# Performance work log

Measured on AMD Instinct MI355X. Metric: run time of the kernel, lower is better.

## Reference

```python
import jax, jax.numpy as jnp
import numpy as np

B, T, DM = 2, 2048, 2048
HQ, HKV, D = 16, 4, 128
MULT = 0.08838834764831845  # attn_output_multiplier = 1/sqrt(key_size)
ROPE_BASE = 10000.0


def rotate_half(x):
    x1, x2 = jnp.split(x, 2, axis=-1)
    return jnp.concatenate((-x2, x1), axis=-1)


def rope_tables(seq_len, dim, dtype):
    inv_freq = 1.0 / (ROPE_BASE ** (jnp.arange(0, dim, 2, dtype=jnp.float32) / dim))
    t = jnp.arange(seq_len, dtype=jnp.float32)
    freqs = jnp.outer(t, inv_freq)              # [T, D/2]
    emb = jnp.concatenate((freqs, freqs), axis=-1)  # [T, D]
    cos = jnp.cos(emb)[None, :, None, :].astype(dtype)  # [1, T, 1, D]
    sin = jnp.sin(emb)[None, :, None, :].astype(dtype)
    return cos, sin


def setup_inputs() -> dict:
    key = jax.random.key(0)
    ks = jax.random.split(key, 5)
    s = 1.0 / np.sqrt(DM)
    x = jax.random.normal(ks[0], (B, T, DM), dtype=jnp.float32)
    Wq = jax.random.normal(ks[1], (DM, HQ * D), dtype=jnp.float32) * s
    Wk = jax.random.normal(ks[2], (DM, HKV * D), dtype=jnp.float32) * s
    Wv = jax.random.normal(ks[3], (DM, HKV * D), dtype=jnp.float32) * s
    Wo = jax.random.normal(ks[4], (HQ * D, DM), dtype=jnp.float32) * s
    mask = jnp.tril(jnp.ones((T, T), dtype=bool))[None, None]  # [1,1,T,T] causal
    return {"x": x, "mask": mask, "Wq": Wq, "Wk": Wk, "Wv": Wv, "Wo": Wo}


def reference(x, mask, Wq, Wk, Wv, Wo):
    Bx, Tx, _ = x.shape
    q = (x @ Wq).reshape(Bx, Tx, HQ, D)
    k = (x @ Wk).reshape(Bx, Tx, HKV, D)
    v = (x @ Wv).reshape(Bx, Tx, HKV, D)
    cos, sin = rope_tables(Tx, D, x.dtype)
    q = q * cos + rotate_half(q) * sin
    k = k * cos + rotate_half(k) * sin
    n_rep = HQ // HKV
    k = jnp.repeat(k, n_rep, axis=2)  # [B,T,HQ,D] (repeat_interleave)
    v = jnp.repeat(v, n_rep, axis=2)
    logits = jnp.einsum('bqhd,bkhd->bhqk', q, k) * MULT
    logits = jnp.where(mask, logits, jnp.float32(-jnp.inf))
    attn = jax.nn.softmax(logits.astype(jnp.float32), axis=-1).astype(x.dtype)
    out = jnp.einsum('bhqk,bkhd->bqhd', attn, v).reshape(Bx, Tx, HQ * D)
    return out @ Wo
```

## Files before the change

kernel.cpp:

```cpp
#include <hip/hip_runtime.h>
#include <cstdint>
#include <cstddef>

#define T_SEQ 2048
#define DMODEL 2048
#define HQ 16
#define HKV 4
#define HD 128

typedef __attribute__((ext_vector_type(4))) float f32x4;
typedef __attribute__((ext_vector_type(8))) short bf16x8;
typedef __attribute__((ext_vector_type(4))) short short4v;
typedef __attribute__((ext_vector_type(2))) short short2v;
typedef __attribute__((ext_vector_type(4))) unsigned uint4v;

__device__ __forceinline__ short f2bf(float f) {
  unsigned u = __builtin_bit_cast(unsigned, f);
  u = (u + 0x7FFFu + ((u >> 16) & 1u)) >> 16;
  return (short)u;
}
__device__ __forceinline__ float bf2f(short s) {
  unsigned u = ((unsigned)(unsigned short)s) << 16;
  return __builtin_bit_cast(float, u);
}
__device__ __forceinline__ unsigned pk_hi16(float a, float b) {
  return __builtin_amdgcn_perm(__builtin_bit_cast(unsigned, b),
                               __builtin_bit_cast(unsigned, a), 0x07060302u);
}

__device__ __forceinline__ void g2lds16(const void* g, void* l) {
  __builtin_amdgcn_global_load_lds(
      (const __attribute__((address_space(1))) void*)g,
      (__attribute__((address_space(3))) void*)l, 16, 0, 0);
}

__global__ void prep_kernel(const float* __restrict__ s0, const float* __restrict__ s1,
                            const float* __restrict__ s2, const float* __restrict__ s3,
                            const float* __restrict__ xs,
                            short* __restrict__ d0, short* __restrict__ d1,
                            short* __restrict__ d2, short* __restrict__ d3,
                            short* __restrict__ xd) {
  const int z = blockIdx.z;
  const int tx = threadIdx.x, ty = threadIdx.y;
  if (z == 4) {
    int bid = blockIdx.y * 64 + blockIdx.x;
    int tid = ty * 32 + tx;
    size_t base = ((size_t)bid * 256 + tid) * 8;
    float4 v0 = *(const float4*)(xs + base);
    float4 v1 = *(const float4*)(xs + base + 4);
    short4v o0, o1;
    o0[0] = f2bf(v0.x); o0[1] = f2bf(v0.y); o0[2] = f2bf(v0.z); o0[3] = f2bf(v0.w);
    o1[0] = f2bf(v1.x); o1[1] = f2bf(v1.y); o1[2] = f2bf(v1.z); o1[3] = f2bf(v1.w);
    *(short4v*)(xd + base) = o0;
    *(short4v*)(xd + base + 4) = o1;
    return;
  }
  __shared__ float tile[32][33];
  const float* src = (z == 0) ? s0 : (z == 1) ? s1 : (z == 2) ? s2 : s3;
  short* dst = (z == 0) ? d0 : (z == 1) ? d1 : (z == 2) ? d2 : d3;
  const int C = (z == 1 || z == 2) ? 512 : 2048;
  const int R = 2048;
  int c0 = blockIdx.x * 32, r0 = blockIdx.y * 32;
  if (c0 >= C) return;
  #pragma unroll
  for (int i = 0; i < 32; i += 8)
    tile[ty + i][tx] = src[(size_t)(r0 + ty + i) * C + c0 + tx];
  __syncthreads();
  #pragma unroll
  for (int i = 0; i < 32; i += 8)
    dst[(size_t)(c0 + ty + i) * R + r0 + tx] = f2bf(tile[tx][ty + i]);
}

template <int MODE>
__global__ __launch_bounds__(256, 2) void gemm_kernel(
    const short* __restrict__ A, const short* __restrict__ BT,
    void* __restrict__ C0, void* __restrict__ C1, void* __restrict__ C2,
    int M, int N, int K)
{
  __shared__ short As[128 * 64];
  __shared__ short Bs[128 * 64];
  const int tid = threadIdx.x;
  const int lane = tid & 63, w = tid >> 6;
  const int l15 = lane & 15, g = lane >> 4;

  const int nbx = gridDim.x;
  const int lid = blockIdx.y * nbx + blockIdx.x;
  const int nwg = nbx * gridDim.y;
  const int cpx = nwg >> 3;
  const int swz = (lid & 7) * cpx + (lid >> 3);
  const int m0 = (swz / nbx) * 128, n0 = (swz % nbx) * 128;

  const int wm = (w >> 1) * 64;
  const int wn32 = (w & 1) * 32;

  const int srow = tid >> 3;
  const int sc   = tid & 7;

  f32x4 acc[4][4] = {};

  for (int k0 = 0; k0 < K; k0 += 64) {
    __syncthreads();
    #pragma unroll
    for (int call = 0; call < 4; call++) {
      int row = call * 32 + srow;
      int csw = sc ^ (row & 7);
      g2lds16(A + (size_t)(m0 + row) * K + k0 + csw * 8,
              (char*)As + call * 4096 + w * 1024);
      g2lds16(BT + (size_t)(n0 + row) * K + k0 + csw * 8,
              (char*)Bs + call * 4096 + w * 1024);
    }
    __syncthreads();
    #pragma unroll
    for (int kk = 0; kk < 2; kk++) {
      bf16x8 af[4], bfr[4];
      #pragma unroll
      for (int mi = 0; mi < 4; mi++) {
        int row = wm + mi * 16 + l15;
        int ch = (kk * 4 + g) ^ (row & 7);
        af[mi] = *(const bf16x8*)(As + row * 64 + ch * 8);
      }
      #pragma unroll
      for (int ni = 0; ni < 4; ni++) {
        int row = wn32 + (ni & 1) * 16 + (ni >> 1) * 64 + l15;
        int ch = (kk * 4 + g) ^ (row & 7);
        bfr[ni] = *(const bf16x8*)(Bs + row * 64 + ch * 8);
      }
      #pragma unroll
      for (int mi = 0; mi < 4; mi++)
        #pragma unroll
        for (int ni = 0; ni < 4; ni++)
          acc[mi][ni] = __builtin_amdgcn_mfma_f32_16x16x32_bf16(af[mi], bfr[ni], acc[mi][ni], 0, 0, 0);
    }
  }

  if (MODE == 1) {
    float* C = (float*)C0;
    #pragma unroll
    for (int mi = 0; mi < 4; mi++)
      #pragma unroll
      for (int r = 0; r < 4; r++) {
        int m = m0 + wm + mi * 16 + g * 4 + r;
        #pragma unroll
        for (int ni = 0; ni < 4; ni++) {
          int col = n0 + wn32 + (ni & 1) * 16 + (ni >> 1) * 64 + l15;
          C[(size_t)m * N + col] = acc[mi][ni][r];
        }
      }
  } else {
    short* Cb; int ldc, nc, rmode;
    if (n0 < 2048)      { Cb = (short*)C0; ldc = 2048; nc = n0;        rmode = 2; }
    else if (n0 < 2560) { Cb = (short*)C1; ldc = 512;  nc = n0 - 2048; rmode = 1; }
    else                { Cb = (short*)C2; ldc = 512;  nc = n0 - 2560; rmode = 0; }

    if (rmode) {
      const float scale = (rmode == 2) ? 0.12754448602243686f
                                       : 1.0f;
      #pragma unroll
      for (int np = 0; np < 2; np++) {
        int i = wn32 + np * 16 + l15;
        float invf = exp2f(-(float)i * 0.20762050593046014f);
        #pragma unroll
        for (int mi = 0; mi < 4; mi++)
          #pragma unroll
          for (int r = 0; r < 4; r++) {
            int m = m0 + wm + mi * 16 + g * 4 + r;
            float theta = (float)(m & 2047) * invf;
            float sn, cs;
            __sincosf(theta, &sn, &cs);
            float lo = acc[mi][np][r], hi = acc[mi][np + 2][r];
            Cb[(size_t)m * ldc + nc + i]      = f2bf((lo * cs - hi * sn) * scale);
            Cb[(size_t)m * ldc + nc + 64 + i] = f2bf((hi * cs + lo * sn) * scale);
          }
      }
    } else {
      #pragma unroll
      for (int mi = 0; mi < 4; mi++)
        #pragma unroll
        for (int r = 0; r < 4; r++) {
          int m = m0 + wm + mi * 16 + g * 4 + r;
          #pragma unroll
          for (int ni = 0; ni < 4; ni++) {
            int col = nc + wn32 + (ni & 1) * 16 + (ni >> 1) * 64 + l15;
            Cb[(size_t)m * ldc + col] = f2bf(acc[mi][ni][r]);
          }
        }
    }
  }
}

__global__ __launch_bounds__(512, 4) void attn_kernel(
    const short* __restrict__ qg, const short* __restrict__ kg,
    const short* __restrict__ vg, short* __restrict__ og)
{
  __shared__ short Ks[2][64 * 128];
  __shared__ short Vt[128 * 64];
  const int tid = threadIdx.x;
  const int lane = tid & 63, w = tid >> 6;
  const int l15 = lane & 15, g = lane >> 4;
  const int b = blockIdx.z;
  const int qti = b ? (15 - (int)blockIdx.x) : (int)blockIdx.x;
  const int qt0 = qti * 128;
  const int h = blockIdx.y, hk = h >> 2;
  const int qw0 = qt0 + w * 16;

  bf16x8 qf[4];
  {
    size_t t = (size_t)b * T_SEQ + qw0 + l15;
    const short* qp = qg + (t * HQ + h) * HD;
    #pragma unroll
    for (int ks = 0; ks < 4; ks++)
      qf[ks] = *(const bf16x8*)(qp + ks * 32 + g * 8);
  }

  f32x4 of[8] = {};
  float m2 = -INFINITY;
  float ls = 0.f;

  const short* kbase = kg + ((size_t)b * T_SEQ * HKV + hk) * HD;
  const short* vbase = vg + ((size_t)b * T_SEQ * HKV + hk) * HD;

  const int kv2 = (tid & 31) * 2;
  const int d8s = (tid >> 5) * 8;
  const int p0 = (kv2 >> 5) * 32 + ((kv2 & 15) >> 2) * 8 + ((kv2 >> 4) & 1) * 4 + (kv2 & 3);
  const int nt = (qt0 + 128) >> 6;

  bf16x8 vr[2];

  auto stageK = [&](int t, int nb) {
    #pragma unroll
    for (int call = 0; call < 2; call++) {
      int tau = call * 512 + tid;
      int kv = tau >> 4, c = tau & 15;
      g2lds16(kbase + (size_t)(t * 64 + kv) * (HKV * HD) + ((c ^ (kv & 7)) << 3),
              (char*)Ks[nb] + call * 8192 + w * 1024);
    }
  };
  auto loadV = [&](int t) {
    const short* vp = vbase + (size_t)(t * 64 + kv2) * (HKV * HD) + d8s;
    vr[0] = *(const bf16x8*)(vp);
    vr[1] = *(const bf16x8*)(vp + HKV * HD);
  };
  auto writeV = [&]() {
    #pragma unroll
    for (int e = 0; e < 8; e++) {
      int row = d8s + e;
      int addr = row * 64 + (((p0 >> 3) ^ e) << 3) + (p0 & 7);
      short2v t2; t2[0] = vr[0][e]; t2[1] = vr[1][e];
      *(short2v*)(&Vt[addr]) = t2;
    }
  };

  stageK(0, 0);
  loadV(0);
  __syncthreads();
  writeV();
  __syncthreads();

  int cur = 0;
  for (int t = 0; t < nt; t++) {
    const int kv0 = t * 64;
    const bool haveNext = (t + 1 < nt);
    if (haveNext) { loadV(t + 1); stageK(t + 1, cur ^ 1); }

    if (kv0 <= qw0 + 15) {
      const short* Kc = Ks[cur];
      f32x4 sacc[4] = {};
      __builtin_amdgcn_s_setprio(1);
      #pragma unroll
      for (int ks = 0; ks < 4; ks++) {
        bf16x8 kf[4];
        #pragma unroll
        for (int kt = 0; kt < 4; kt++) {
          int row = kt * 16 + l15;
          int ch = (ks * 4 + g) ^ (row & 7);
          kf[kt] = *(const bf16x8*)(Kc + row * 128 + ch * 8);
        }
        #pragma unroll
        for (int kt = 0; kt < 4; kt++)
          sacc[kt] = __builtin_amdgcn_mfma_f32_16x16x32_bf16(kf[kt], qf[ks], sacc[kt], 0, 0, 0);
      }
      __builtin_amdgcn_s_setprio(0);
      const bool needmask = (kv0 + 63) > qw0;
      const int qpos = qw0 + l15;
      float vmax = -INFINITY;
      #pragma unroll
      for (int kt = 0; kt < 4; kt++)
        #pragma unroll
        for (int r = 0; r < 4; r++) {
          int kvpos = kv0 + kt * 16 + g * 4 + r;
          float sv = sacc[kt][r];
          if (needmask && kvpos > qpos) sv = -INFINITY;
          sacc[kt][r] = sv;
          vmax = fmaxf(vmax, sv);
        }
      vmax = fmaxf(vmax, __shfl_xor(vmax, 16));
      vmax = fmaxf(vmax, __shfl_xor(vmax, 32));
      if (!__all(vmax <= m2 + 8.0f)) {
        float mnew = fmaxf(m2, vmax);
        float resc = exp2f(m2 - mnew);
        m2 = mnew;
        ls *= resc;
        #pragma unroll
        for (int dc = 0; dc < 8; dc++) of[dc] *= resc;
      }
      #pragma unroll
      for (int kt = 0; kt < 4; kt++)
        #pragma unroll
        for (int r = 0; r < 4; r++) {
          float p = exp2f(sacc[kt][r] - m2);
          sacc[kt][r] = p;
          ls += p;
        }
      bf16x8 pb[2];
      #pragma unroll
      for (int ktw = 0; ktw < 2; ktw++) {
        uint4v pw;
        pw[0] = pk_hi16(sacc[2 * ktw][0], sacc[2 * ktw][1]);
        pw[1] = pk_hi16(sacc[2 * ktw][2], sacc[2 * ktw][3]);
        pw[2] = pk_hi16(sacc[2 * ktw + 1][0], sacc[2 * ktw + 1][1]);
        pw[3] = pk_hi16(sacc[2 * ktw + 1][2], sacc[2 * ktw + 1][3]);
        pb[ktw] = __builtin_bit_cast(bf16x8, pw);
      }
      __builtin_amdgcn_s_setprio(1);
      #pragma unroll
      for (int ktw = 0; ktw < 2; ktw++)
        #pragma unroll
        for (int dc = 0; dc < 8; dc++) {
          int row = dc * 16 + l15;
          bf16x8 vf = *(const bf16x8*)(&Vt[row * 64 + ((ktw * 32 + g * 8) ^ ((l15 & 7) << 3))]);
          of[dc] = __builtin_amdgcn_mfma_f32_16x16x32_bf16(vf, pb[ktw], of[dc], 0, 0, 0);
        }
      __builtin_amdgcn_s_setprio(0);
    }

    __syncthreads();
    if (haveNext) writeV();
    __syncthreads();
    cur ^= 1;
  }

  {
    ls += __shfl_xor(ls, 16);
    ls += __shfl_xor(ls, 32);
    float inv = 1.0f / ls;
    size_t t = (size_t)b * T_SEQ + qw0 + l15;
    short* op = og + (t * HQ + h) * HD;
    #pragma unroll
    for (int dc = 0; dc < 8; dc++) {
      short4v o;
      #pragma unroll
      for (int r = 0; r < 4; r++) o[r] = f2bf(of[dc][r] * inv);
      *(short4v*)(op + dc * 16 + g * 4) = o;
    }
  }
}

extern "C" void kernel_launch(void* const* d_in, const int* in_sizes, int n_in,
                              void* d_out, int out_size, void* d_ws, size_t ws_size,
                              hipStream_t stream) {
  (void)in_sizes; (void)n_in; (void)out_size; (void)ws_size;
  const float* x  = (const float*)d_in[0];
  const float* Wq = (const float*)d_in[2];
  const float* Wk = (const float*)d_in[3];
  const float* Wv = (const float*)d_in[4];
  const float* Wo = (const float*)d_in[5];

  char* ws = (char*)d_ws;
  short* xb   = (short*)(ws);
  short* wall = (short*)(ws + 16777216);
  short* wkT  = wall + (size_t)2048 * 2048;
  short* wvT  = wall + (size_t)2560 * 2048;
  short* woT  = (short*)(ws + 29360128);
  short* qb   = (short*)(ws + 37748736);
  short* kb   = (short*)(ws + 54525952);
  short* vb   = (short*)(ws + 58720256);
  short* ab   = (short*)(ws + 62914560);

  dim3 tb(32, 8);
  prep_kernel<<<dim3(64, 64, 5), tb, 0, stream>>>(Wq, Wk, Wv, Wo, x,
                                                  wall, wkT, wvT, woT, xb);

  gemm_kernel<2><<<dim3(24, 32), 256, 0, stream>>>(xb, wall, qb, kb, vb, 4096, 3072, 2048);

  attn_kernel<<<dim3(16, 16, 2), 512, 0, stream>>>(qb, kb, vb, ab);

  gemm_kernel<1><<<dim3(16, 32), 256, 0, stream>>>(ab, woT, d_out, nullptr, nullptr, 4096, 2048, 2048);
}
```

Measured before the change: 190.9 us.

## Split attention KV range across two blocks with 256-row query tiles and combine

Each attention block now handles 256 query rows, with every wave processing two 16-row query chunks so each K/V tile in LDS is reused twice. The KV tiles are split by parity between two blocks (split-KV), and a new combine kernel merges the two partial outputs using their saved max and sum statistics. The intent is to raise K/V reuse per LDS load while keeping the same grid size and balancing causal work. The cost is an extra kernel launch and partial-output traffic through reused workspace, and higher register pressure, which is why the occupancy hint drops from 4 to 2.

```diff
diff --git a/kernel.cpp b/kernel.cpp
--- a/kernel.cpp
+++ b/kernel.cpp
@@ -188,9 +188,10 @@
   }
 }
 
-__global__ __launch_bounds__(512, 4) void attn_kernel(
+__global__ __launch_bounds__(512, 2) void attn_kernel(
     const short* __restrict__ qg, const short* __restrict__ kg,
-    const short* __restrict__ vg, short* __restrict__ og)
+    const short* __restrict__ vg, short* __restrict__ og,
+    short* __restrict__ pOn, float2* __restrict__ ml)
 {
   __shared__ short Ks[2][64 * 128];
   __shared__ short Vt[128 * 64];
@@ -198,23 +199,25 @@
   const int lane = tid & 63, w = tid >> 6;
   const int l15 = lane & 15, g = lane >> 4;
   const int b = blockIdx.z;
-  const int qti = b ? (15 - (int)blockIdx.x) : (int)blockIdx.x;
-  const int qt0 = qti * 128;
+  const int qx = blockIdx.x >> 1, hf = blockIdx.x & 1;
+  const int qti = b ? (7 - qx) : qx;
+  const int qt0 = qti * 256;
   const int h = blockIdx.y, hk = h >> 2;
-  const int qw0 = qt0 + w * 16;
-
-  bf16x8 qf[4];
-  {
-    size_t t = (size_t)b * T_SEQ + qw0 + l15;
+  const int qw0 = qt0 + w * 32;
+
+  bf16x8 qf[2][4];
+  #pragma unroll
+  for (int qc = 0; qc < 2; qc++) {
+    size_t t = (size_t)b * T_SEQ + qw0 + qc * 16 + l15;
     const short* qp = qg + (t * HQ + h) * HD;
     #pragma unroll
     for (int ks = 0; ks < 4; ks++)
-      qf[ks] = *(const bf16x8*)(qp + ks * 32 + g * 8);
-  }
-
-  f32x4 of[8] = {};
-  float m2 = -INFINITY;
-  float ls = 0.f;
+      qf[qc][ks] = *(const bf16x8*)(qp + ks * 32 + g * 8);
+  }
+
+  f32x4 of[2][8] = {};
+  float m2[2] = {-INFINITY, -INFINITY};
+  float ls[2] = {0.f, 0.f};
 
   const short* kbase = kg + ((size_t)b * T_SEQ * HKV + hk) * HD;
   const short* vbase = vg + ((size_t)b * T_SEQ * HKV + hk) * HD;
@@ -222,7 +225,7 @@
   const int kv2 = (tid & 31) * 2;
   const int d8s = (tid >> 5) * 8;
   const int p0 = (kv2 >> 5) * 32 + ((kv2 & 15) >> 2) * 8 + ((kv2 >> 4) & 1) * 4 + (kv2 & 3);
-  const int nt = (qt0 + 128) >> 6;
+  const int ntAll = 4 * qti + 4;
 
   bf16x8 vr[2];
 
@@ -250,21 +253,22 @@
     }
   };
 
-  stageK(0, 0);
-  loadV(0);
+  stageK(hf, 0);
+  loadV(hf);
   __syncthreads();
   writeV();
   __syncthreads();
 
-  int cur = 0;
-  for (int t = 0; t < nt; t++) {
+  int buf = 0;
+  for (int t = hf; t < ntAll; t += 2) {
     const int kv0 = t * 64;
-    const bool haveNext = (t + 1 < nt);
-    if (haveNext) { loadV(t + 1); stageK(t + 1, cur ^ 1); }
-
-    if (kv0 <= qw0 + 15) {
-      const short* Kc = Ks[cur];
-      f32x4 sacc[4] = {};
+    const int tn = t + 2;
+    const bool haveNext = (tn < ntAll);
+    if (haveNext) { loadV(tn); stageK(tn, buf ^ 1); }
+
+    if (kv0 <= qw0 + 31) {
+      const short* Kc = Ks[buf];
+      f32x4 sacc[4][2] = {};
       __builtin_amdgcn_s_setprio(1);
       #pragma unroll
       for (int ks = 0; ks < 4; ks++) {
@@ -277,49 +281,55 @@
         }
         #pragma unroll
         for (int kt = 0; kt < 4; kt++)
-          sacc[kt] = __builtin_amdgcn_mfma_f32_16x16x32_bf16(kf[kt], qf[ks], sacc[kt], 0, 0, 0);
+          #pragma unroll
+          for (int qc = 0; qc < 2; qc++)
+            sacc[kt][qc] = __builtin_amdgcn_mfma_f32_16x16x32_bf16(kf[kt], qf[qc][ks], sacc[kt][qc], 0, 0, 0);
       }
       __builtin_amdgcn_s_setprio(0);
       const bool needmask = (kv0 + 63) > qw0;
-      const int qpos = qw0 + l15;
-      float vmax = -INFINITY;
-      #pragma unroll
-      for (int kt = 0; kt < 4; kt++)
-        #pragma unroll
-        for (int r = 0; r < 4; r++) {
-          int kvpos = kv0 + kt * 16 + g * 4 + r;
-          float sv = sacc[kt][r];
-          if (needmask && kvpos > qpos) sv = -INFINITY;
-          sacc[kt][r] = sv;
-          vmax = fmaxf(vmax, sv);
-        }
-      vmax = fmaxf(vmax, __shfl_xor(vmax, 16));
-      vmax = fmaxf(vmax, __shfl_xor(vmax, 32));
-      if (!__all(vmax <= m2 + 8.0f)) {
-        float mnew = fmaxf(m2, vmax);
-        float resc = exp2f(m2 - mnew);
-        m2 = mnew;
-        ls *= resc;
-        #pragma unroll
-        for (int dc = 0; dc < 8; dc++) of[dc] *= resc;
-      }
-      #pragma unroll
-      for (int kt = 0; kt < 4; kt++)
-        #pragma unroll
-        for (int r = 0; r < 4; r++) {
-          float p = exp2f(sacc[kt][r] - m2);
-          sacc[kt][r] = p;
-          ls += p;
-        }
-      bf16x8 pb[2];
-      #pragma unroll
-      for (int ktw = 0; ktw < 2; ktw++) {
-        uint4v pw;
-        pw[0] = pk_hi16(sacc[2 * ktw][0], sacc[2 * ktw][1]);
-        pw[1] = pk_hi16(sacc[2 * ktw][2], sacc[2 * ktw][3]);
-        pw[2] = pk_hi16(sacc[2 * ktw + 1][0], sacc[2 * ktw + 1][1]);
-        pw[3] = pk_hi16(sacc[2 * ktw + 1][2], sacc[2 * ktw + 1][3]);
-        pb[ktw] = __builtin_bit_cast(bf16x8, pw);
+      bf16x8 pb[2][2];
+      #pragma unroll
+      for (int qc = 0; qc < 2; qc++) {
+        int qpos = qw0 + qc * 16 + l15;
+        float vmax = -INFINITY;
+        #pragma unroll
+        for (int kt = 0; kt < 4; kt++)
+          #pragma unroll
+          for (int r = 0; r < 4; r++) {
+            int kvpos = kv0 + kt * 16 + g * 4 + r;
+            float sv = sacc[kt][qc][r];
+            if (needmask && kvpos > qpos) sv = -INFINITY;
+            sacc[kt][qc][r] = sv;
+            vmax = fmaxf(vmax, sv);
+          }
+        vmax = fmaxf(vmax, __shfl_xor(vmax, 16));
+        vmax = fmaxf(vmax, __shfl_xor(vmax, 32));
+        if (!__all(vmax <= m2[qc] + 8.0f)) {
+          float mnew = fmaxf(m2[qc], vmax);
+          float resc = exp2f(m2[qc] - mnew);
+          m2[qc] = mnew;
+          ls[qc] *= resc;
+          #pragma unroll
+          for (int dc = 0; dc < 8; dc++) of[qc][dc] *= resc;
+        }
+        float mref = m2[qc];
+        #pragma unroll
+        for (int kt = 0; kt < 4; kt++)
+          #pragma unroll
+          for (int r = 0; r < 4; r++) {
+            float p = exp2f(sacc[kt][qc][r] - mref);
+            sacc[kt][qc][r] = p;
+            ls[qc] += p;
+          }
+        #pragma unroll
+        for (int ktw = 0; ktw < 2; ktw++) {
+          uint4v pw;
+          pw[0] = pk_hi16(sacc[2 * ktw][qc][0], sacc[2 * ktw][qc][1]);
+          pw[1] = pk_hi16(sacc[2 * ktw][qc][2], sacc[2 * ktw][qc][3]);
+          pw[2] = pk_hi16(sacc[2 * ktw + 1][qc][0], sacc[2 * ktw + 1][qc][1]);
+          pw[3] = pk_hi16(sacc[2 * ktw + 1][qc][2], sacc[2 * ktw + 1][qc][3]);
+          pb[ktw][qc] = __builtin_bit_cast(bf16x8, pw);
+        }
       }
       __builtin_amdgcn_s_setprio(1);
       #pragma unroll
@@ -328,7 +338,9 @@
         for (int dc = 0; dc < 8; dc++) {
           int row = dc * 16 + l15;
           bf16x8 vf = *(const bf16x8*)(&Vt[row * 64 + ((ktw * 32 + g * 8) ^ ((l15 & 7) << 3))]);
-          of[dc] = __builtin_amdgcn_mfma_f32_16x16x32_bf16(vf, pb[ktw], of[dc], 0, 0, 0);
+          #pragma unroll
+          for (int qc = 0; qc < 2; qc++)
+            of[qc][dc] = __builtin_amdgcn_mfma_f32_16x16x32_bf16(vf, pb[ktw][qc], of[qc][dc], 0, 0, 0);
         }
       __builtin_amdgcn_s_setprio(0);
     }
@@ -336,23 +348,53 @@
     __syncthreads();
     if (haveNext) writeV();
     __syncthreads();
-    cur ^= 1;
-  }
-
-  {
-    ls += __shfl_xor(ls, 16);
-    ls += __shfl_xor(ls, 32);
-    float inv = 1.0f / ls;
-    size_t t = (size_t)b * T_SEQ + qw0 + l15;
-    short* op = og + (t * HQ + h) * HD;
+    buf ^= 1;
+  }
+
+  #pragma unroll
+  for (int qc = 0; qc < 2; qc++) {
+    float lss = ls[qc];
+    lss += __shfl_xor(lss, 16);
+    lss += __shfl_xor(lss, 32);
+    float inv = lss > 0.f ? 1.0f / lss : 0.f;
+    const int q = qw0 + qc * 16 + l15;
+    size_t row = (size_t)(b * 16 + h) * 2048 + q;
+    short* op = (hf == 0) ? (og + (((size_t)b * T_SEQ + q) * HQ + h) * HD)
+                          : (pOn + row * 128);
     #pragma unroll
     for (int dc = 0; dc < 8; dc++) {
       short4v o;
       #pragma unroll
-      for (int r = 0; r < 4; r++) o[r] = f2bf(of[dc][r] * inv);
+      for (int r = 0; r < 4; r++) o[r] = f2bf(of[qc][dc][r] * inv);
       *(short4v*)(op + dc * 16 + g * 4) = o;
     }
-  }
+    if (g == 0) {
+      float2 st; st.x = m2[qc]; st.y = lss;
+      ml[(size_t)hf * 65536 + row] = st;
+    }
+  }
+}
+
+__global__ void combine_kernel(const short* __restrict__ pOn, const float2* __restrict__ ml,
+                               short* __restrict__ ab) {
+  int idx = blockIdx.x * 256 + threadIdx.x;
+  int d4 = (idx & 31) * 4;
+  int r = idx >> 5;
+  int q = r & 2047, bh = r >> 11;
+  float2 s0 = ml[r], s1 = ml[65536 + r];
+  float M = fmaxf(s0.x, s1.x);
+  float w0 = s0.y * exp2f(s0.x - M);
+  float w1 = s1.y * exp2f(s1.x - M);
+  float inv = 1.0f / (w0 + w1);
+  w0 *= inv; w1 *= inv;
+  int bb = bh >> 4, hh = bh & 15;
+  size_t aoff = ((size_t)(bb * T_SEQ + q) * HQ + hh) * HD + d4;
+  short4v a = *(const short4v*)(ab + aoff);
+  short4v c = *(const short4v*)(pOn + (size_t)r * 128 + d4);
+  short4v o;
+  #pragma unroll
+  for (int j = 0; j < 4; j++) o[j] = f2bf(w0 * bf2f(a[j]) + w1 * bf2f(c[j]));
+  *(short4v*)(ab + aoff) = o;
 }
 
 extern "C" void kernel_launch(void* const* d_in, const int* in_sizes, int n_in,
@@ -366,15 +408,17 @@
   const float* Wo = (const float*)d_in[5];
 
   char* ws = (char*)d_ws;
-  short* xb   = (short*)(ws);
-  short* wall = (short*)(ws + 16777216);
-  short* wkT  = wall + (size_t)2048 * 2048;
-  short* wvT  = wall + (size_t)2560 * 2048;
-  short* woT  = (short*)(ws + 29360128);
-  short* qb   = (short*)(ws + 37748736);
-  short* kb   = (short*)(ws + 54525952);
-  short* vb   = (short*)(ws + 58720256);
-  short* ab   = (short*)(ws + 62914560);
+  short*  xb   = (short*)(ws);
+  short*  wall = (short*)(ws + 16777216);
+  short*  wkT  = wall + (size_t)2048 * 2048;
+  short*  wvT  = wall + (size_t)2560 * 2048;
+  short*  pOn  = (short*)(ws);
+  float2* ml   = (float2*)(ws + 16777216);
+  short*  woT  = (short*)(ws + 29360128);
+  short*  qb   = (short*)(ws + 37748736);
+  short*  kb   = (short*)(ws + 54525952);
+  short*  vb   = (short*)(ws + 58720256);
+  short*  ab   = (short*)(ws + 62914560);
 
   dim3 tb(32, 8);
   prep_kernel<<<dim3(64, 64, 5), tb, 0, stream>>>(Wq, Wk, Wv, Wo, x,
@@ -382,7 +426,8 @@
 
   gemm_kernel<2><<<dim3(24, 32), 256, 0, stream>>>(xb, wall, qb, kb, vb, 4096, 3072, 2048);
 
-  attn_kernel<<<dim3(16, 16, 2), 512, 0, stream>>>(qb, kb, vb, ab);
+  attn_kernel<<<dim3(16, 16, 2), 512, 0, stream>>>(qb, kb, vb, ab, pOn, ml);
+  combine_kernel<<<8192, 256, 0, stream>>>(pOn, ml, ab);
 
   gemm_kernel<1><<<dim3(16, 32), 256, 0, stream>>>(ab, woT, d_out, nullptr, nullptr, 4096, 2048, 2048);
 }
```

Result: slower. 221.4 us (+16.0%).
